# Performance work log

Hardware: AMD Instinct MI355X
Metric: run time of the kernel (lower is better)

## Reference

```python
import jax, jax.numpy as jnp
import numpy as np

DIM = 1024
DIM_HEADS = 64  # number of heads in this module (per-head dim is 1, see source quirk)


def setup_inputs() -> dict:
    key = jax.random.key(0)
    k1, k2, k3 = jax.random.split(key, 3)
    x = jax.random.normal(k1, (1, 2048, DIM), dtype=jnp.float32)
    # torch Linear weight layout: [out_features, in_features]
    w_qkv = jax.random.normal(k2, (DIM_HEADS * 3, DIM), dtype=jnp.float32) * 0.02
    w_out = jax.random.normal(k3, (DIM, DIM_HEADS), dtype=jnp.float32) * 0.02
    return {"x": x, "w_qkv": w_qkv, "w_out": w_out}


def reference(x, w_qkv, w_out):
    b, n, _ = x.shape
    h = DIM_HEADS
    qkv = jnp.einsum('bnc,fc->bnf', x, w_qkv)          # [b, n, 3*h]
    q, k, v = jnp.split(qkv, 3, axis=-1)                # each [b, n, h]
    # rearrange 'b n (h d) -> b h n d' with h = DIM_HEADS => d = 1
    q = q.transpose(0, 2, 1)[..., None]                 # [b, h, n, 1]
    k = k.transpose(0, 2, 1)[..., None]
    v = v.transpose(0, 2, 1)[..., None]
    scale = 1.0 / jnp.sqrt(jnp.float32(h))              # source divides by sqrt(dim_heads)
    dots = jnp.einsum('bhid,bhjd->bhij', q, k) * scale  # [b, h, n, n]
    causal = jnp.tril(jnp.ones((n, n), dtype=bool))
    dots = jnp.where(causal, dots, -jnp.inf)
    attn = jax.nn.softmax(dots, axis=-1)
    out = jnp.einsum('bhij,bhjd->bhid', attn, v)        # [b, h, n, 1]
    out = out[..., 0].transpose(0, 2, 1)                # [b, n, h]
    return jnp.einsum('bnh,ch->bnc', out, w_out)        # [b, n, dim]
```

## Files before the change

kernel.cpp:

```cpp
#include <hip/hip_runtime.h>


__global__ void transpose_kernel(const float* __restrict__ in, float* __restrict__ out,
                                 int rows, int cols) {
    int idx = blockIdx.x * 256 + threadIdx.x;
    int total = rows * cols;
    if (idx < total) {
        int r = idx / cols;
        int c = idx - r * cols;
        out[c * rows + r] = in[idx];
    }
}

__global__ __launch_bounds__(256) void qkv_gemm(const float* __restrict__ x,
                                                const float* __restrict__ wT,
                                                float* __restrict__ pq) {
    __shared__ float xsT[32][64];
    __shared__ float wsld[32][64];
    const int t = threadIdx.x;
    const int b = blockIdx.x;
    const int ks = b & 3;
    const int nt = (b >> 2) % 3;
    const int mt = b / 12;
    const int i0 = mt * 64;
    const int cb = nt * 64;
    const int k0 = ks * 256;

    const int rf = t & 63;
    const int kq = t >> 6;
    const int tx = t & 15;
    const int ty = t >> 4;

    const float* xp = x + (size_t)(i0 + rf) * 1024 + k0 + kq * 8;
    const float* wp = wT + (size_t)(k0 + kq * 8) * 192 + cb + rf;

    float4 xa = *(const float4*)(xp);
    float4 xb = *(const float4*)(xp + 4);
    float wr[8];
#pragma unroll
    for (int j = 0; j < 8; ++j) wr[j] = wp[(size_t)j * 192];

    float acc[4][4] = {};

    for (int s = 0; s < 8; ++s) {
        __syncthreads();
        {
            const int kb = kq * 8;
            xsT[kb + 0][rf] = xa.x; xsT[kb + 1][rf] = xa.y;
            xsT[kb + 2][rf] = xa.z; xsT[kb + 3][rf] = xa.w;
            xsT[kb + 4][rf] = xb.x; xsT[kb + 5][rf] = xb.y;
            xsT[kb + 6][rf] = xb.z; xsT[kb + 7][rf] = xb.w;
#pragma unroll
            for (int j = 0; j < 8; ++j) wsld[kb + j][rf] = wr[j];
        }
        __syncthreads();
        if (s < 7) {
            const float* xp2 = xp + (s + 1) * 32;
            xa = *(const float4*)(xp2);
            xb = *(const float4*)(xp2 + 4);
            const float* wp2 = wp + (size_t)(s + 1) * 32 * 192;
#pragma unroll
            for (int j = 0; j < 8; ++j) wr[j] = wp2[(size_t)j * 192];
        }
#pragma unroll
        for (int k = 0; k < 32; ++k) {
            float4 a4 = *(const float4*)&xsT[k][ty * 4];
            float4 b4 = *(const float4*)&wsld[k][tx * 4];
            acc[0][0] = fmaf(a4.x, b4.x, acc[0][0]);
            acc[0][1] = fmaf(a4.x, b4.y, acc[0][1]);
            acc[0][2] = fmaf(a4.x, b4.z, acc[0][2]);
            acc[0][3] = fmaf(a4.x, b4.w, acc[0][3]);
            acc[1][0] = fmaf(a4.y, b4.x, acc[1][0]);
            acc[1][1] = fmaf(a4.y, b4.y, acc[1][1]);
            acc[1][2] = fmaf(a4.y, b4.z, acc[1][2]);
            acc[1][3] = fmaf(a4.y, b4.w, acc[1][3]);
            acc[2][0] = fmaf(a4.z, b4.x, acc[2][0]);
            acc[2][1] = fmaf(a4.z, b4.y, acc[2][1]);
            acc[2][2] = fmaf(a4.z, b4.z, acc[2][2]);
            acc[2][3] = fmaf(a4.z, b4.w, acc[2][3]);
            acc[3][0] = fmaf(a4.w, b4.x, acc[3][0]);
            acc[3][1] = fmaf(a4.w, b4.y, acc[3][1]);
            acc[3][2] = fmaf(a4.w, b4.z, acc[3][2]);
            acc[3][3] = fmaf(a4.w, b4.w, acc[3][3]);
        }
    }

    float* pbase = pq + (size_t)ks * 192 * 2048 + (size_t)cb * 2048 + i0;
#pragma unroll
    for (int cc = 0; cc < 4; ++cc) {
        float4 o = make_float4(acc[0][cc], acc[1][cc], acc[2][cc], acc[3][cc]);
        *(float4*)(pbase + (size_t)(tx * 4 + cc) * 2048 + ty * 4) = o;
    }
}

__global__ __launch_bounds__(256) void qkv_reduce(const float* __restrict__ pq,
                                                  float* __restrict__ qws,
                                                  float* __restrict__ skws,
                                                  float* __restrict__ vws) {
    const int idx = blockIdx.x * 256 + threadIdx.x;
    const int f = idx >> 9;
    const int i = (idx & 511) * 4;
    const size_t S = (size_t)192 * 2048;
    const size_t o = (size_t)f * 2048 + i;
    float4 a0 = *(const float4*)(pq + o);
    float4 a1 = *(const float4*)(pq + S + o);
    float4 a2 = *(const float4*)(pq + 2 * S + o);
    float4 a3 = *(const float4*)(pq + 3 * S + o);
    const int which = f >> 6;
    const float sc = (which == 1) ? 0.125f : 1.0f;
    float4 r = make_float4((a0.x + a1.x + a2.x + a3.x) * sc,
                           (a0.y + a1.y + a2.y + a3.y) * sc,
                           (a0.z + a1.z + a2.z + a3.z) * sc,
                           (a0.w + a1.w + a2.w + a3.w) * sc);
    float* dst = (which == 0) ? qws : (which == 1) ? skws : vws;
    *(float4*)(dst + (size_t)(f & 63) * 2048 + i) = r;
}

__global__ __launch_bounds__(256) void attn_kernel(const float* __restrict__ qws,
                                                   const float* __restrict__ skws,
                                                   const float* __restrict__ vws,
                                                   float* __restrict__ pn,
                                                   float* __restrict__ pd) {
    const int c = threadIdx.x >> 6;
    const int lane = threadIdx.x & 63;
    const int u = blockIdx.x;
    const int h = u & 63;
    const int rb = 31 - (u >> 6);
    const int i = rb * 64 + lane;

    const float* skp = skws + (size_t)h * 2048;
    const float* vp  = vws  + (size_t)h * 2048;
    const float qv = qws[(size_t)h * 2048 + i];

    const int qlen = (rb + 1) * 16;
    const int jstart = c * qlen;
    const int jend = jstart + qlen;
    const int diag = rb * 64;
    const int bend = (jend < diag) ? jend : diag;
    const int mstart = (jstart > diag) ? jstart : diag;

    float den0 = 0.f, den1 = 0.f, den2 = 0.f, den3 = 0.f;
    float num0 = 0.f, num1 = 0.f, num2 = 0.f, num3 = 0.f;

    for (int j = jstart; j < bend; j += 8) {
        float4 s0 = *(const float4*)(skp + j);
        float4 s1 = *(const float4*)(skp + j + 4);
        float4 v0 = *(const float4*)(vp + j);
        float4 v1 = *(const float4*)(vp + j + 4);
        float e;
        e = __expf(qv * s0.x); den0 += e; num0 = fmaf(e, v0.x, num0);
        e = __expf(qv * s0.y); den1 += e; num1 = fmaf(e, v0.y, num1);
        e = __expf(qv * s0.z); den2 += e; num2 = fmaf(e, v0.z, num2);
        e = __expf(qv * s0.w); den3 += e; num3 = fmaf(e, v0.w, num3);
        e = __expf(qv * s1.x); den0 += e; num0 = fmaf(e, v1.x, num0);
        e = __expf(qv * s1.y); den1 += e; num1 = fmaf(e, v1.y, num1);
        e = __expf(qv * s1.z); den2 += e; num2 = fmaf(e, v1.z, num2);
        e = __expf(qv * s1.w); den3 += e; num3 = fmaf(e, v1.w, num3);
    }
    for (int j = mstart; j < jend; j += 8) {
        float4 s0 = *(const float4*)(skp + j);
        float4 s1 = *(const float4*)(skp + j + 4);
        float4 v0 = *(const float4*)(vp + j);
        float4 v1 = *(const float4*)(vp + j + 4);
        float e;
        e = (j     <= i) ? __expf(qv * s0.x) : 0.f; den0 += e; num0 = fmaf(e, v0.x, num0);
        e = (j + 1 <= i) ? __expf(qv * s0.y) : 0.f; den1 += e; num1 = fmaf(e, v0.y, num1);
        e = (j + 2 <= i) ? __expf(qv * s0.z) : 0.f; den2 += e; num2 = fmaf(e, v0.z, num2);
        e = (j + 3 <= i) ? __expf(qv * s0.w) : 0.f; den3 += e; num3 = fmaf(e, v0.w, num3);
        e = (j + 4 <= i) ? __expf(qv * s1.x) : 0.f; den0 += e; num0 = fmaf(e, v1.x, num0);
        e = (j + 5 <= i) ? __expf(qv * s1.y) : 0.f; den1 += e; num1 = fmaf(e, v1.y, num1);
        e = (j + 6 <= i) ? __expf(qv * s1.z) : 0.f; den2 += e; num2 = fmaf(e, v1.z, num2);
        e = (j + 7 <= i) ? __expf(qv * s1.w) : 0.f; den3 += e; num3 = fmaf(e, v1.w, num3);
    }
    const size_t o = (size_t)(c * 64 + h) * 2048 + i;
    pn[o] = (num0 + num1) + (num2 + num3);
    pd[o] = (den0 + den1) + (den2 + den3);
}

__global__ __launch_bounds__(256) void attn_reduce(const float* __restrict__ pn,
                                                   const float* __restrict__ pd,
                                                   float* __restrict__ aws) {
    const int idx = blockIdx.x * 256 + threadIdx.x;
    const int h = idx >> 9;
    const int i = (idx & 511) * 4;
    const size_t S = (size_t)64 * 2048;
    const size_t o = (size_t)h * 2048 + i;
    float4 n0 = *(const float4*)(pn + o);
    float4 n1 = *(const float4*)(pn + S + o);
    float4 n2 = *(const float4*)(pn + 2 * S + o);
    float4 n3 = *(const float4*)(pn + 3 * S + o);
    float4 d0 = *(const float4*)(pd + o);
    float4 d1 = *(const float4*)(pd + S + o);
    float4 d2 = *(const float4*)(pd + 2 * S + o);
    float4 d3 = *(const float4*)(pd + 3 * S + o);
    float4 r = make_float4(((n0.x + n1.x) + (n2.x + n3.x)) / ((d0.x + d1.x) + (d2.x + d3.x)),
                           ((n0.y + n1.y) + (n2.y + n3.y)) / ((d0.y + d1.y) + (d2.y + d3.y)),
                           ((n0.z + n1.z) + (n2.z + n3.z)) / ((d0.z + d1.z) + (d2.z + d3.z)),
                           ((n0.w + n1.w) + (n2.w + n3.w)) / ((d0.w + d1.w) + (d2.w + d3.w)));
    *(float4*)(aws + o) = r;
}

__global__ __launch_bounds__(256) void proj_kernel(const float* __restrict__ aws,
                                                   const float* __restrict__ wOutT,
                                                   float* __restrict__ out) {
    __shared__ float ast[64][17];
    const int t = threadIdx.x;
    const int i0 = (blockIdx.x >> 3) * 16;
    const int c0 = (blockIdx.x & 7) * 128;

    {
        const int h = t >> 2, iq = t & 3;
        float4 v = *(const float4*)(aws + (size_t)h * 2048 + i0 + iq * 4);
        ast[h][iq * 4 + 0] = v.x; ast[h][iq * 4 + 1] = v.y;
        ast[h][iq * 4 + 2] = v.z; ast[h][iq * 4 + 3] = v.w;
    }
    __syncthreads();

    const int rg = t >> 5;
    const int cg = t & 31;
    const float* wp = wOutT + c0 + cg * 4;
    float acc[2][4] = {};
#pragma unroll 8
    for (int hc = 0; hc < 64; ++hc) {
        float4 w4 = *(const float4*)(wp + (size_t)hc * 1024);
        float a0 = ast[hc][rg * 2];
        float a1 = ast[hc][rg * 2 + 1];
        acc[0][0] = fmaf(a0, w4.x, acc[0][0]);
        acc[0][1] = fmaf(a0, w4.y, acc[0][1]);
        acc[0][2] = fmaf(a0, w4.z, acc[0][2]);
        acc[0][3] = fmaf(a0, w4.w, acc[0][3]);
        acc[1][0] = fmaf(a1, w4.x, acc[1][0]);
        acc[1][1] = fmaf(a1, w4.y, acc[1][1]);
        acc[1][2] = fmaf(a1, w4.z, acc[1][2]);
        acc[1][3] = fmaf(a1, w4.w, acc[1][3]);
    }
#pragma unroll
    for (int rr = 0; rr < 2; ++rr) {
        *(float4*)(out + (size_t)(i0 + rg * 2 + rr) * 1024 + c0 + cg * 4) =
            make_float4(acc[rr][0], acc[rr][1], acc[rr][2], acc[rr][3]);
    }
}

extern "C" void kernel_launch(void* const* d_in, const int* in_sizes, int n_in,
                              void* d_out, int out_size, void* d_ws, size_t ws_size,
                              hipStream_t stream) {
    const float* x     = (const float*)d_in[0];
    const float* w_qkv = (const float*)d_in[1];
    const float* w_out = (const float*)d_in[2];
    float* out = (float*)d_out;

    float* ws    = (float*)d_ws;
    float* wT    = ws;
    float* wOutT = wT + 196608;
    float* pq    = wOutT + 65536;
    float* qws   = pq + 1572864;
    float* skws  = qws + 131072;
    float* vws   = skws + 131072;
    float* pn    = vws + 131072;
    float* pd    = pn + 524288;
    float* aws   = pd + 524288;

    transpose_kernel<<<dim3(768), dim3(256), 0, stream>>>(w_qkv, wT, 192, 1024);
    transpose_kernel<<<dim3(256), dim3(256), 0, stream>>>(w_out, wOutT, 1024, 64);
    qkv_gemm<<<dim3(384), dim3(256), 0, stream>>>(x, wT, pq);
    qkv_reduce<<<dim3(384), dim3(256), 0, stream>>>(pq, qws, skws, vws);
    attn_kernel<<<dim3(2048), dim3(256), 0, stream>>>(qws, skws, vws, pn, pd);
    attn_reduce<<<dim3(128), dim3(256), 0, stream>>>(pn, pd, aws);
    proj_kernel<<<dim3(1024), dim3(256), 0, stream>>>(aws, wOutT, out);
}
```

Measured before the change: 135.5 us.

## Fuse pipeline into four kernels with atomic split-K, paired causal rows, exp2

```diff
diff --git a/kernel.cpp b/kernel.cpp
--- a/kernel.cpp
+++ b/kernel.cpp
@@ -1,30 +1,50 @@
 #include <hip/hip_runtime.h>
 
 
-__global__ void transpose_kernel(const float* __restrict__ in, float* __restrict__ out,
-                                 int rows, int cols) {
-    int idx = blockIdx.x * 256 + threadIdx.x;
-    int total = rows * cols;
-    if (idx < total) {
-        int r = idx / cols;
-        int c = idx - r * cols;
-        out[c * rows + r] = in[idx];
+#if __has_builtin(__builtin_amdgcn_exp2f)
+#define EXP2F(x) __builtin_amdgcn_exp2f(x)
+#else
+#define EXP2F(x) exp2f(x)
+#endif
+
+#define LOG2E_DIV8 0.18033688011112042f
+
+__global__ __launch_bounds__(256) void prep_kernel(const float* __restrict__ wqkv,
+                                                   const float* __restrict__ wout,
+                                                   float* __restrict__ wT,
+                                                   float* __restrict__ wOutT,
+                                                   float* __restrict__ qsv) {
+    const int b = blockIdx.x;
+    if (b < 768) {
+        int idx = b * 256 + threadIdx.x;
+        int f = idx >> 10, k = idx & 1023;
+        float val = wqkv[idx];
+        if (f >= 64 && f < 128) val *= LOG2E_DIV8;
+        wT[k * 192 + f] = val;
+    } else if (b < 1024) {
+        int idx = (b - 768) * 256 + threadIdx.x;
+        int cc = idx >> 6, hh = idx & 63;
+        wOutT[hh * 1024 + cc] = wout[idx];
+    } else {
+        int idx = (b - 1024) * 256 + threadIdx.x;
+        float4 z = make_float4(0.f, 0.f, 0.f, 0.f);
+        ((float4*)qsv)[idx] = z;
     }
 }
 
 __global__ __launch_bounds__(256) void qkv_gemm(const float* __restrict__ x,
                                                 const float* __restrict__ wT,
-                                                float* __restrict__ pq) {
+                                                float* __restrict__ qsv) {
     __shared__ float xsT[32][64];
     __shared__ float wsld[32][64];
     const int t = threadIdx.x;
     const int b = blockIdx.x;
-    const int ks = b & 3;
-    const int nt = (b >> 2) % 3;
-    const int mt = b / 12;
+    const int ks = b & 7;
+    const int nt = (b >> 3) % 3;
+    const int mt = b / 24;
     const int i0 = mt * 64;
     const int cb = nt * 64;
-    const int k0 = ks * 256;
+    const int k0 = ks * 128;
 
     const int rf = t & 63;
     const int kq = t >> 6;
@@ -42,7 +62,7 @@
 
     float acc[4][4] = {};
 
-    for (int s = 0; s < 8; ++s) {
+    for (int s = 0; s < 4; ++s) {
         __syncthreads();
         {
             const int kb = kq * 8;
@@ -54,7 +74,7 @@
             for (int j = 0; j < 8; ++j) wsld[kb + j][rf] = wr[j];
         }
         __syncthreads();
-        if (s < 7) {
+        if (s < 3) {
             const float* xp2 = xp + (s + 1) * 32;
             xa = *(const float4*)(xp2);
             xb = *(const float4*)(xp2 + 4);
@@ -85,160 +105,161 @@
         }
     }
 
-    float* pbase = pq + (size_t)ks * 192 * 2048 + (size_t)cb * 2048 + i0;
 #pragma unroll
     for (int cc = 0; cc < 4; ++cc) {
-        float4 o = make_float4(acc[0][cc], acc[1][cc], acc[2][cc], acc[3][cc]);
-        *(float4*)(pbase + (size_t)(tx * 4 + cc) * 2048 + ty * 4) = o;
-    }
-}
-
-__global__ __launch_bounds__(256) void qkv_reduce(const float* __restrict__ pq,
-                                                  float* __restrict__ qws,
-                                                  float* __restrict__ skws,
-                                                  float* __restrict__ vws) {
-    const int idx = blockIdx.x * 256 + threadIdx.x;
-    const int f = idx >> 9;
-    const int i = (idx & 511) * 4;
-    const size_t S = (size_t)192 * 2048;
-    const size_t o = (size_t)f * 2048 + i;
-    float4 a0 = *(const float4*)(pq + o);
-    float4 a1 = *(const float4*)(pq + S + o);
-    float4 a2 = *(const float4*)(pq + 2 * S + o);
-    float4 a3 = *(const float4*)(pq + 3 * S + o);
-    const int which = f >> 6;
-    const float sc = (which == 1) ? 0.125f : 1.0f;
-    float4 r = make_float4((a0.x + a1.x + a2.x + a3.x) * sc,
-                           (a0.y + a1.y + a2.y + a3.y) * sc,
-                           (a0.z + a1.z + a2.z + a3.z) * sc,
-                           (a0.w + a1.w + a2.w + a3.w) * sc);
-    float* dst = (which == 0) ? qws : (which == 1) ? skws : vws;
-    *(float4*)(dst + (size_t)(f & 63) * 2048 + i) = r;
-}
-
-__global__ __launch_bounds__(256) void attn_kernel(const float* __restrict__ qws,
-                                                   const float* __restrict__ skws,
-                                                   const float* __restrict__ vws,
+        const int f = cb + tx * 4 + cc;
+        const int which = f >> 6;
+        const int h = f & 63;
+        float* dst = qsv + (size_t)which * 131072 + (size_t)h * 2048 + i0 + ty * 4;
+#pragma unroll
+        for (int rr = 0; rr < 4; ++rr) atomicAdd(dst + rr, acc[rr][cc]);
+    }
+}
+
+__global__ __launch_bounds__(256) void attn_kernel(const float* __restrict__ qsv,
                                                    float* __restrict__ pn,
                                                    float* __restrict__ pd) {
-    const int c = threadIdx.x >> 6;
-    const int lane = threadIdx.x & 63;
-    const int u = blockIdx.x;
-    const int h = u & 63;
-    const int rb = 31 - (u >> 6);
-    const int i = rb * 64 + lane;
-
-    const float* skp = skws + (size_t)h * 2048;
-    const float* vp  = vws  + (size_t)h * 2048;
-    const float qv = qws[(size_t)h * 2048 + i];
-
-    const int qlen = (rb + 1) * 16;
-    const int jstart = c * qlen;
-    const int jend = jstart + qlen;
-    const int diag = rb * 64;
-    const int bend = (jend < diag) ? jend : diag;
-    const int mstart = (jstart > diag) ? jstart : diag;
-
-    float den0 = 0.f, den1 = 0.f, den2 = 0.f, den3 = 0.f;
-    float num0 = 0.f, num1 = 0.f, num2 = 0.f, num3 = 0.f;
-
-    for (int j = jstart; j < bend; j += 8) {
-        float4 s0 = *(const float4*)(skp + j);
-        float4 s1 = *(const float4*)(skp + j + 4);
-        float4 v0 = *(const float4*)(vp + j);
-        float4 v1 = *(const float4*)(vp + j + 4);
-        float e;
-        e = __expf(qv * s0.x); den0 += e; num0 = fmaf(e, v0.x, num0);
-        e = __expf(qv * s0.y); den1 += e; num1 = fmaf(e, v0.y, num1);
-        e = __expf(qv * s0.z); den2 += e; num2 = fmaf(e, v0.z, num2);
-        e = __expf(qv * s0.w); den3 += e; num3 = fmaf(e, v0.w, num3);
-        e = __expf(qv * s1.x); den0 += e; num0 = fmaf(e, v1.x, num0);
-        e = __expf(qv * s1.y); den1 += e; num1 = fmaf(e, v1.y, num1);
-        e = __expf(qv * s1.z); den2 += e; num2 = fmaf(e, v1.z, num2);
-        e = __expf(qv * s1.w); den3 += e; num3 = fmaf(e, v1.w, num3);
-    }
-    for (int j = mstart; j < jend; j += 8) {
-        float4 s0 = *(const float4*)(skp + j);
-        float4 s1 = *(const float4*)(skp + j + 4);
-        float4 v0 = *(const float4*)(vp + j);
-        float4 v1 = *(const float4*)(vp + j + 4);
-        float e;
-        e = (j     <= i) ? __expf(qv * s0.x) : 0.f; den0 += e; num0 = fmaf(e, v0.x, num0);
-        e = (j + 1 <= i) ? __expf(qv * s0.y) : 0.f; den1 += e; num1 = fmaf(e, v0.y, num1);
-        e = (j + 2 <= i) ? __expf(qv * s0.z) : 0.f; den2 += e; num2 = fmaf(e, v0.z, num2);
-        e = (j + 3 <= i) ? __expf(qv * s0.w) : 0.f; den3 += e; num3 = fmaf(e, v0.w, num3);
-        e = (j + 4 <= i) ? __expf(qv * s1.x) : 0.f; den0 += e; num0 = fmaf(e, v1.x, num0);
-        e = (j + 5 <= i) ? __expf(qv * s1.y) : 0.f; den1 += e; num1 = fmaf(e, v1.y, num1);
-        e = (j + 6 <= i) ? __expf(qv * s1.z) : 0.f; den2 += e; num2 = fmaf(e, v1.z, num2);
-        e = (j + 7 <= i) ? __expf(qv * s1.w) : 0.f; den3 += e; num3 = fmaf(e, v1.w, num3);
-    }
-    const size_t o = (size_t)(c * 64 + h) * 2048 + i;
-    pn[o] = (num0 + num1) + (num2 + num3);
-    pd[o] = (den0 + den1) + (den2 + den3);
-}
-
-__global__ __launch_bounds__(256) void attn_reduce(const float* __restrict__ pn,
+    __shared__ float ssk[2048];
+    __shared__ float svv[2048];
+    const int t = threadIdx.x;
+    const int h = blockIdx.x & 63;
+    const int p = blockIdx.x >> 6;
+    const int lane = t & 63;
+    const int c = t >> 6;
+
+    const int Alen = (p + 1) * 64;
+    const int L    = (32 - p) * 64;
+    const float* skp = qsv + 131072 + (size_t)h * 2048;
+    const float* vp  = qsv + 262144 + (size_t)h * 2048;
+
+    for (int idx = t * 4; idx < L; idx += 1024) {
+        *(float4*)&ssk[idx] = *(const float4*)(skp + idx);
+        *(float4*)&svv[idx] = *(const float4*)(vp + idx);
+    }
+    __syncthreads();
+
+    const int i1 = Alen - 64 + lane;
+    const int i2 = L - 64 + lane;
+    const float qv1 = qsv[(size_t)h * 2048 + i1];
+    const float qv2 = qsv[(size_t)h * 2048 + i2];
+
+    float dA[4] = {0.f, 0.f, 0.f, 0.f}, nA[4] = {0.f, 0.f, 0.f, 0.f};
+    float dB[4] = {0.f, 0.f, 0.f, 0.f}, nB[4] = {0.f, 0.f, 0.f, 0.f};
+
+    const int gs = c * 528, ge = gs + 528;
+
+    if (gs < Alen) {
+        const int a1 = (ge < Alen) ? ge : Alen;
+        const int d1 = Alen - 64;
+        const int be = (a1 < d1) ? a1 : d1;
+        for (int j = gs; j < be; j += 16) {
+#pragma unroll
+            for (int u = 0; u < 4; ++u) {
+                float4 s = *(const float4*)&ssk[j + 4 * u];
+                float4 v = *(const float4*)&svv[j + 4 * u];
+                float e0 = EXP2F(qv1 * s.x), e1 = EXP2F(qv1 * s.y);
+                float e2 = EXP2F(qv1 * s.z), e3 = EXP2F(qv1 * s.w);
+                dA[0] += e0; nA[0] = fmaf(e0, v.x, nA[0]);
+                dA[1] += e1; nA[1] = fmaf(e1, v.y, nA[1]);
+                dA[2] += e2; nA[2] = fmaf(e2, v.z, nA[2]);
+                dA[3] += e3; nA[3] = fmaf(e3, v.w, nA[3]);
+            }
+        }
+        const int ms = (gs > d1) ? gs : d1;
+        for (int j = ms; j < a1; j += 16) {
+#pragma unroll
+            for (int u = 0; u < 4; ++u) {
+                float4 s = *(const float4*)&ssk[j + 4 * u];
+                float4 v = *(const float4*)&svv[j + 4 * u];
+                const int jb = j + 4 * u;
+                float e0 = (jb     <= i1) ? EXP2F(qv1 * s.x) : 0.f;
+                float e1 = (jb + 1 <= i1) ? EXP2F(qv1 * s.y) : 0.f;
+                float e2 = (jb + 2 <= i1) ? EXP2F(qv1 * s.z) : 0.f;
+                float e3 = (jb + 3 <= i1) ? EXP2F(qv1 * s.w) : 0.f;
+                dA[0] += e0; nA[0] = fmaf(e0, v.x, nA[0]);
+                dA[1] += e1; nA[1] = fmaf(e1, v.y, nA[1]);
+                dA[2] += e2; nA[2] = fmaf(e2, v.z, nA[2]);
+                dA[3] += e3; nA[3] = fmaf(e3, v.w, nA[3]);
+            }
+        }
+    }
+
+    if (ge > Alen) {
+        const int b0 = ((gs > Alen) ? gs : Alen) - Alen;
+        const int b1 = ge - Alen;
+        const int d2 = L - 64;
+        const int be = (b1 < d2) ? b1 : d2;
+        for (int j = b0; j < be; j += 16) {
+#pragma unroll
+            for (int u = 0; u < 4; ++u) {
+                float4 s = *(const float4*)&ssk[j + 4 * u];
+                float4 v = *(const float4*)&svv[j + 4 * u];
+                float e0 = EXP2F(qv2 * s.x), e1 = EXP2F(qv2 * s.y);
+                float e2 = EXP2F(qv2 * s.z), e3 = EXP2F(qv2 * s.w);
+                dB[0] += e0; nB[0] = fmaf(e0, v.x, nB[0]);
+                dB[1] += e1; nB[1] = fmaf(e1, v.y, nB[1]);
+                dB[2] += e2; nB[2] = fmaf(e2, v.z, nB[2]);
+                dB[3] += e3; nB[3] = fmaf(e3, v.w, nB[3]);
+            }
+        }
+        const int ms = (b0 > d2) ? b0 : d2;
+        for (int j = ms; j < b1; j += 16) {
+#pragma unroll
+            for (int u = 0; u < 4; ++u) {
+                float4 s = *(const float4*)&ssk[j + 4 * u];
+                float4 v = *(const float4*)&svv[j + 4 * u];
+                const int jb = j + 4 * u;
+                float e0 = (jb     <= i2) ? EXP2F(qv2 * s.x) : 0.f;
+                float e1 = (jb + 1 <= i2) ? EXP2F(qv2 * s.y) : 0.f;
+                float e2 = (jb + 2 <= i2) ? EXP2F(qv2 * s.z) : 0.f;
+                float e3 = (jb + 3 <= i2) ? EXP2F(qv2 * s.w) : 0.f;
+                dB[0] += e0; nB[0] = fmaf(e0, v.x, nB[0]);
+                dB[1] += e1; nB[1] = fmaf(e1, v.y, nB[1]);
+                dB[2] += e2; nB[2] = fmaf(e2, v.z, nB[2]);
+                dB[3] += e3; nB[3] = fmaf(e3, v.w, nB[3]);
+            }
+        }
+    }
+
+    const size_t base = ((size_t)c * 64 + h) * 2048;
+    pn[base + i1] = (nA[0] + nA[1]) + (nA[2] + nA[3]);
+    pd[base + i1] = (dA[0] + dA[1]) + (dA[2] + dA[3]);
+    pn[base + i2] = (nB[0] + nB[1]) + (nB[2] + nB[3]);
+    pd[base + i2] = (dB[0] + dB[1]) + (dB[2] + dB[3]);
+}
+
+__global__ __launch_bounds__(256) void proj_kernel(const float* __restrict__ pn,
                                                    const float* __restrict__ pd,
-                                                   float* __restrict__ aws) {
-    const int idx = blockIdx.x * 256 + threadIdx.x;
-    const int h = idx >> 9;
-    const int i = (idx & 511) * 4;
-    const size_t S = (size_t)64 * 2048;
-    const size_t o = (size_t)h * 2048 + i;
-    float4 n0 = *(const float4*)(pn + o);
-    float4 n1 = *(const float4*)(pn + S + o);
-    float4 n2 = *(const float4*)(pn + 2 * S + o);
-    float4 n3 = *(const float4*)(pn + 3 * S + o);
-    float4 d0 = *(const float4*)(pd + o);
-    float4 d1 = *(const float4*)(pd + S + o);
-    float4 d2 = *(const float4*)(pd + 2 * S + o);
-    float4 d3 = *(const float4*)(pd + 3 * S + o);
-    float4 r = make_float4(((n0.x + n1.x) + (n2.x + n3.x)) / ((d0.x + d1.x) + (d2.x + d3.x)),
-                           ((n0.y + n1.y) + (n2.y + n3.y)) / ((d0.y + d1.y) + (d2.y + d3.y)),
-                           ((n0.z + n1.z) + (n2.z + n3.z)) / ((d0.z + d1.z) + (d2.z + d3.z)),
-                           ((n0.w + n1.w) + (n2.w + n3.w)) / ((d0.w + d1.w) + (d2.w + d3.w)));
-    *(float4*)(aws + o) = r;
-}
-
-__global__ __launch_bounds__(256) void proj_kernel(const float* __restrict__ aws,
                                                    const float* __restrict__ wOutT,
                                                    float* __restrict__ out) {
-    __shared__ float ast[64][17];
+    __shared__ float ast[64][8];
     const int t = threadIdx.x;
-    const int i0 = (blockIdx.x >> 3) * 16;
+    const int i0 = (blockIdx.x >> 3) * 8;
     const int c0 = (blockIdx.x & 7) * 128;
 
-    {
-        const int h = t >> 2, iq = t & 3;
-        float4 v = *(const float4*)(aws + (size_t)h * 2048 + i0 + iq * 4);
-        ast[h][iq * 4 + 0] = v.x; ast[h][iq * 4 + 1] = v.y;
-        ast[h][iq * 4 + 2] = v.z; ast[h][iq * 4 + 3] = v.w;
+    for (int s = t; s < 512; s += 256) {
+        const int hh = s >> 3, ii = s & 7;
+        const size_t o = (size_t)hh * 2048 + i0 + ii;
+        float n = (pn[o] + pn[131072 + o]) + (pn[262144 + o] + pn[393216 + o]);
+        float d = (pd[o] + pd[131072 + o]) + (pd[262144 + o] + pd[393216 + o]);
+        ast[hh][ii] = n / d;
     }
     __syncthreads();
 
     const int rg = t >> 5;
     const int cg = t & 31;
     const float* wp = wOutT + c0 + cg * 4;
-    float acc[2][4] = {};
+    float a0 = 0.f, a1 = 0.f, a2 = 0.f, a3 = 0.f;
 #pragma unroll 8
     for (int hc = 0; hc < 64; ++hc) {
         float4 w4 = *(const float4*)(wp + (size_t)hc * 1024);
-        float a0 = ast[hc][rg * 2];
-        float a1 = ast[hc][rg * 2 + 1];
-        acc[0][0] = fmaf(a0, w4.x, acc[0][0]);
-        acc[0][1] = fmaf(a0, w4.y, acc[0][1]);
-        acc[0][2] = fmaf(a0, w4.z, acc[0][2]);
-        acc[0][3] = fmaf(a0, w4.w, acc[0][3]);
-        acc[1][0] = fmaf(a1, w4.x, acc[1][0]);
-        acc[1][1] = fmaf(a1, w4.y, acc[1][1]);
-        acc[1][2] = fmaf(a1, w4.z, acc[1][2]);
-        acc[1][3] = fmaf(a1, w4.w, acc[1][3]);
-    }
-#pragma unroll
-    for (int rr = 0; rr < 2; ++rr) {
-        *(float4*)(out + (size_t)(i0 + rg * 2 + rr) * 1024 + c0 + cg * 4) =
-            make_float4(acc[rr][0], acc[rr][1], acc[rr][2], acc[rr][3]);
-    }
+        float a = ast[hc][rg];
+        a0 = fmaf(a, w4.x, a0);
+        a1 = fmaf(a, w4.y, a1);
+        a2 = fmaf(a, w4.z, a2);
+        a3 = fmaf(a, w4.w, a3);
+    }
+    *(float4*)(out + (size_t)(i0 + rg) * 1024 + c0 + cg * 4) = make_float4(a0, a1, a2, a3);
 }
 
 extern "C" void kernel_launch(void* const* d_in, const int* in_sizes, int n_in,
@@ -252,19 +273,12 @@
     float* ws    = (float*)d_ws;
     float* wT    = ws;
     float* wOutT = wT + 196608;
-    float* pq    = wOutT + 65536;
-    float* qws   = pq + 1572864;
-    float* skws  = qws + 131072;
-    float* vws   = skws + 131072;
-    float* pn    = vws + 131072;
+    float* qsv   = wOutT + 65536;
+    float* pn    = qsv + 393216;
     float* pd    = pn + 524288;
-    float* aws   = pd + 524288;
-
-    transpose_kernel<<<dim3(768), dim3(256), 0, stream>>>(w_qkv, wT, 192, 1024);
-    transpose_kernel<<<dim3(256), dim3(256), 0, stream>>>(w_out, wOutT, 1024, 64);
-    qkv_gemm<<<dim3(384), dim3(256), 0, stream>>>(x, wT, pq);
-    qkv_reduce<<<dim3(384), dim3(256), 0, stream>>>(pq, qws, skws, vws);
-    attn_kernel<<<dim3(2048), dim3(256), 0, stream>>>(qws, skws, vws, pn, pd);
-    attn_reduce<<<dim3(128), dim3(256), 0, stream>>>(pn, pd, aws);
-    proj_kernel<<<dim3(1024), dim3(256), 0, stream>>>(aws, wOutT, out);
-}
+
+    prep_kernel<<<dim3(1408), dim3(256), 0, stream>>>(w_qkv, w_out, wT, wOutT, qsv);
+    qkv_gemm<<<dim3(768), dim3(256), 0, stream>>>(x, wT, qsv);
+    attn_kernel<<<dim3(1024), dim3(256), 0, stream>>>(qsv, pn, pd);
+    proj_kernel<<<dim3(2048), dim3(256), 0, stream>>>(pn, pd, wOutT, out);
+}
```

Measured after the change: 166.1 us. +22.6%, slower.
